# Kernel optimization log

Hardware: AMD Instinct MI355X
Metric: run time of the kernel (lower is better)

The kernel has to match this reference:

```python
import jax, jax.numpy as jnp
import numpy as np

D_MODEL = 1024
N_HEADS = 16  # long-term branch; short/medium use N_HEADS // 2


def _band_bias(seq_len, scale_factor):
    # Intended semantics of create_temporal_mask: position i may attend to
    # positions j >= i - scale_factor (recent past + all future); positions
    # further than scale_factor in the past are blocked.
    i = jnp.arange(seq_len)[:, None]
    j = jnp.arange(seq_len)[None, :]
    return jnp.where(j >= i - scale_factor, 0.0, -1e9).astype(jnp.float32)


def _mha(x, w_in, b_in, w_out, b_out, n_heads, bias):
    # Faithful nn.MultiheadAttention (batch_first, eval/no dropout).
    B, S, D = x.shape
    dk = D // n_heads
    qkv = x @ w_in.T + b_in                       # [B,S,3D]
    q, k, v = jnp.split(qkv, 3, axis=-1)
    def heads(t):
        return t.reshape(B, S, n_heads, dk).transpose(0, 2, 1, 3)  # [B,H,S,dk]
    q, k, v = heads(q), heads(k), heads(v)
    scores = jnp.einsum('bhid,bhjd->bhij', q, k) / np.sqrt(dk).astype(np.float32)
    if bias is not None:
        scores = scores + bias
    attn = jax.nn.softmax(scores, axis=-1)        # [B,H,S,S]
    out = jnp.einsum('bhij,bhjd->bhid', attn, v)  # [B,H,S,dk]
    out = out.transpose(0, 2, 1, 3).reshape(B, S, D)
    return out @ w_out.T + b_out, attn


def _layernorm(x, gamma, beta, eps=1e-5):
    mu = jnp.mean(x, axis=-1, keepdims=True)
    var = jnp.var(x, axis=-1, keepdims=True)
    return (x - mu) * jax.lax.rsqrt(var + eps) * gamma + beta


def setup_inputs() -> dict:
    key = jax.random.key(0)
    ks = jax.random.split(key, 12)
    D = D_MODEL
    s = 0.02
    inp = {
        'x': jax.random.normal(ks[0], (2, 2048, D), dtype=jnp.float32),
        'w_in_s': jax.random.normal(ks[1], (3 * D, D), dtype=jnp.float32) * s,
        'b_in_s': jnp.zeros((3 * D,), dtype=jnp.float32),
        'wo_s': jax.random.normal(ks[2], (D, D), dtype=jnp.float32) * s,
        'bo_s': jnp.zeros((D,), dtype=jnp.float32),
        'w_in_m': jax.random.normal(ks[3], (3 * D, D), dtype=jnp.float32) * s,
        'b_in_m': jnp.zeros((3 * D,), dtype=jnp.float32),
        'wo_m': jax.random.normal(ks[4], (D, D), dtype=jnp.float32) * s,
        'bo_m': jnp.zeros((D,), dtype=jnp.float32),
        'w_in_l': jax.random.normal(ks[5], (3 * D, D), dtype=jnp.float32) * s,
        'b_in_l': jnp.zeros((3 * D,), dtype=jnp.float32),
        'wo_l': jax.random.normal(ks[6], (D, D), dtype=jnp.float32) * s,
        'bo_l': jnp.zeros((D,), dtype=jnp.float32),
        'w_comb': jax.random.normal(ks[7], (D, 3 * D), dtype=jnp.float32) * s,
        'b_comb': jnp.zeros((D,), dtype=jnp.float32),
        'gamma': jnp.ones((D,), dtype=jnp.float32),
        'beta': jnp.zeros((D,), dtype=jnp.float32),
    }
    return inp


def reference(x, w_in_s, b_in_s, wo_s, bo_s,
              w_in_m, b_in_m, wo_m, bo_m,
              w_in_l, b_in_l, wo_l, bo_l,
              w_comb, b_comb, gamma, beta):
    B, S, D = x.shape
    short_bias = _band_bias(S, 10)
    medium_bias = _band_bias(S, 30)
    short_out, _ = _mha(x, w_in_s, b_in_s, wo_s, bo_s, N_HEADS // 2, short_bias)
    medium_out, _ = _mha(x, w_in_m, b_in_m, wo_m, bo_m, N_HEADS // 2, medium_bias)
    long_out, attn = _mha(x, w_in_l, b_in_l, wo_l, bo_l, N_HEADS, None)
    attn_weights = jnp.mean(attn, axis=1)  # torch default average_attn_weights=True -> [B,S,S]
    combined = jnp.concatenate([short_out, medium_out, long_out], axis=-1)
    output = combined @ w_comb.T + b_comb
    return _layernorm(output + x, gamma, beta), attn_weights
```

## Files before the change

kernel.cpp:

```cpp
#include <hip/hip_runtime.h>
#include <hip/hip_bf16.h>
#include <math.h>

#define B_ 2
#define S_ 2048
#define D_ 1024
#define M_ (B_*S_)
#define CTXLD 3072

typedef _Float16 half8_t __attribute__((ext_vector_type(8)));
typedef _Float16 half4_t __attribute__((ext_vector_type(4)));
typedef float    f32x4  __attribute__((ext_vector_type(4)));

#define GL2LDS(g, l) __builtin_amdgcn_global_load_lds( \
    (const __attribute__((address_space(1))) void*)(uintptr_t)(g), \
    (__attribute__((address_space(3))) void*)(l), 16, 0, 0)

#define QSC_L  0.18033688011112043f
#define QSC_SM 0.12751744653921766f

struct GemmBatch {
    const _Float16* A;
    const _Float16* W;
    const float*    bias;
    void*           C;
    void*           C2;
};

template<int MODE, int NB>
__device__ __forceinline__ void gemm_body(
    _Float16* As, _Float16* Bs, const GemmBatch& G,
    int lda, int ldw, int ldc, int K, int bx, int by, int bz)
{
    constexpr int NT = NB / 32;

    const int t = threadIdx.x, lane = t & 63, w = t >> 6;
    const int bm = bx * 128, bn = by * NB;
    const int wm = (w >> 1) * 64, wn = (w & 1) * (NB/2);
    const int fr = lane & 15, q8 = (lane >> 4) * 8;
    const int srow = lane >> 2, scol = (lane & 3) * 8;

    f32x4 acc[4][NT] = {};

    const _Float16* Ab = G.A + (size_t)(bm + w*32 + srow) * lda + scol;
    const _Float16* Wb = G.W + (size_t)(bn + w*(NB/4) + srow) * ldw + scol;

    for (int k0 = 0; k0 < K; k0 += 64) {
        __syncthreads();
        #pragma unroll
        for (int kc = 0; kc < 2; kc++) {
            #pragma unroll
            for (int ii = 0; ii < 2; ii++)
                GL2LDS(Ab + (size_t)(ii*16)*lda + k0 + kc*32,
                       As + kc*4096 + w*1024 + ii*512);
            #pragma unroll
            for (int ii = 0; ii < NB/64; ii++)
                GL2LDS(Wb + (size_t)(ii*16)*ldw + k0 + kc*32,
                       Bs + kc*NB*32 + w*(NB/4)*32 + ii*512);
        }
        __syncthreads();
        #pragma unroll
        for (int kc = 0; kc < 2; kc++) {
            half8_t af[4], bf[NT];
            #pragma unroll
            for (int mt = 0; mt < 4; mt++)
                af[mt] = *(const half8_t*)&As[kc*4096 + (wm + mt*16 + fr)*32 + q8];
            #pragma unroll
            for (int nt = 0; nt < NT; nt++)
                bf[nt] = *(const half8_t*)&Bs[kc*NB*32 + (wn + nt*16 + fr)*32 + q8];
            #pragma unroll
            for (int mt = 0; mt < 4; mt++)
                #pragma unroll
                for (int nt = 0; nt < NT; nt++)
                    acc[mt][nt] = __builtin_amdgcn_mfma_f32_16x16x32_f16(
                        af[mt], bf[nt], acc[mt][nt], 0, 0, 0);
        }
    }

    const int cl = lane & 15;
    const int rq = (lane >> 4) * 4;

    if (MODE == 2 && bn >= 2048) {
        #pragma unroll
        for (int mt = 0; mt < 4; mt++) {
            int row0 = bm + wm + mt*16 + rq;
            #pragma unroll
            for (int nt = 0; nt < NT; nt++) {
                int gcol = bn + wn + nt*16 + cl;
                float bv = G.bias[gcol];
                half4_t hv = {(_Float16)(acc[mt][nt][0] + bv),
                              (_Float16)(acc[mt][nt][1] + bv),
                              (_Float16)(acc[mt][nt][2] + bv),
                              (_Float16)(acc[mt][nt][3] + bv)};
                *(half4_t*)((_Float16*)G.C2 + (size_t)(gcol - 2048) * M_ + row0) = hv;
            }
        }
        return;
    }

    const float qsc = (MODE == 2 && bn < 1024)
                      ? ((bz == 2) ? QSC_L : QSC_SM) : 1.0f;

    #pragma unroll
    for (int mt = 0; mt < 4; mt++) {
        #pragma unroll
        for (int r = 0; r < 4; r++) {
            size_t grow = (size_t)(bm + wm + mt*16 + rq + r);
            #pragma unroll
            for (int nt = 0; nt < NT; nt++) {
                int gcol = bn + wn + nt*16 + cl;
                float v = acc[mt][nt][r] + ((MODE == 3) ? 0.f : G.bias[gcol]);
                if (MODE == 2) v *= qsc;
                if (MODE == 0)
                    ((float*)G.C)[grow * ldc + gcol] = v;
                else
                    ((_Float16*)G.C)[grow * ldc + gcol] = (_Float16)v;
            }
        }
    }
}

template<int MODE, int NB>
__global__ __launch_bounds__(256) void gemm_f16(
    GemmBatch b0, GemmBatch b1, GemmBatch b2, int lda, int ldw, int ldc, int K)
{
    __shared__ __align__(16) _Float16 As[2*128*32];
    __shared__ __align__(16) _Float16 Bs[2*NB*32];
    const GemmBatch G = (blockIdx.z == 0) ? b0 : ((blockIdx.z == 1) ? b1 : b2);
    gemm_body<MODE, NB>(As, Bs, G, lda, ldw, ldc, K,
                        blockIdx.x, blockIdx.y, blockIdx.z);
}

struct CastArgs {
    const float* s[5];
    _Float16*    d[5];
    int          nb[5];
};

__global__ __launch_bounds__(256) void prep_mega(
    CastArgs a,
    const float* wo_s, const float* wo_m, const float* wo_l,
    _Float16* woT_s, _Float16* woT_m, _Float16* woT_l,
    const float* __restrict__ w_comb, const float* __restrict__ b_comb,
    const float* __restrict__ bo_s, const float* __restrict__ bo_m,
    const float* __restrict__ bo_l, float* __restrict__ beff)
{
    __shared__ float T[64][68];
    __shared__ float red[4];
    const int bid = blockIdx.x;

    if (bid < 16384) {
        int off = bid;
        int seg = 0;
        while (seg < 4 && off >= a.nb[seg]) { off -= a.nb[seg]; seg++; }
        int i = off * 256 + threadIdx.x;
        float4 v = ((const float4*)a.s[seg])[i];
        half4_t h = {(_Float16)v.x, (_Float16)v.y, (_Float16)v.z, (_Float16)v.w};
        ((half4_t*)a.d[seg])[i] = h;
        return;
    }
    if (bid < 16384 + 768) {
        int rr0 = bid - 16384;
        int bz = rr0 >> 8, rem = rr0 & 255;
        int bx = rem & 15, by = rem >> 4;
        const float* src = bz == 0 ? wo_s : (bz == 1 ? wo_m : wo_l);
        _Float16*    dst = bz == 0 ? woT_s : (bz == 1 ? woT_m : woT_l);
        const int db = bx * 64;
        const int eb = by * 64;
        const int r = threadIdx.x >> 4;
        const int c = (threadIdx.x & 15) * 4;

        #pragma unroll
        for (int rr = 0; rr < 4; rr++) {
            float4 v = *(const float4*)&src[(size_t)(db + rr*16 + r)*1024 + eb + c];
            T[rr*16 + r][c+0] = v.x; T[rr*16 + r][c+1] = v.y;
            T[rr*16 + r][c+2] = v.z; T[rr*16 + r][c+3] = v.w;
        }
        __syncthreads();
        #pragma unroll
        for (int rr = 0; rr < 4; rr++) {
            int e = rr*16 + r;
            half4_t hv = {(_Float16)T[c+0][e], (_Float16)T[c+1][e],
                          (_Float16)T[c+2][e], (_Float16)T[c+3][e]};
            *(half4_t*)&dst[(size_t)(eb + e)*1024 + db + c] = hv;
        }
        return;
    }
    {
        const int n = bid - (16384 + 768), t = threadIdx.x;
        float s = 0.f;
        for (int d = t; d < 1024; d += 256)
            s += w_comb[(size_t)n*3072 + d]        * bo_s[d]
               + w_comb[(size_t)n*3072 + 1024 + d] * bo_m[d]
               + w_comb[(size_t)n*3072 + 2048 + d] * bo_l[d];
        #pragma unroll
        for (int m = 32; m >= 1; m >>= 1) s += __shfl_xor(s, m);
        if ((t & 63) == 0) red[t >> 6] = s;
        __syncthreads();
        if (t == 0) beff[n] = b_comb[n] + red[0] + red[1] + red[2] + red[3];
    }
}

template<int DK, int BJ, bool LOUT>
__device__ __forceinline__ void flash_body(
    _Float16* lds, float* Lw,
    const _Float16* __restrict__ qk, const _Float16* __restrict__ vT,
    _Float16* __restrict__ ctx, float* __restrict__ lout,
    int window, int b, int h, int qblk, int H)
{
    constexpr int KS  = DK / 32;
    constexpr int DT  = DK / 16;
    constexpr int JT  = BJ / 16;
    constexpr int JC  = BJ / 32;
    constexpr int LDP = 40;

    _Float16* Ks = lds;
    _Float16* Vs = lds + DK*BJ;
    _Float16* Ps = lds + 2*DK*BJ;

    const int t = threadIdx.x, lane = t & 63, w = t >> 6;
    const int fr = lane & 15, g = lane >> 4, k8 = g * 8;
    const int k8s = (g ^ ((fr >> 1) & 3)) * 8;
    const int blkQ = qblk * 64;
    const int qlo  = blkQ + w * 16;

    _Float16* PsW = Ps + w * 16 * LDP;
    const int srow = lane >> 2;
    const int ssw  = ((lane & 3) ^ ((srow >> 1) & 3)) * 8;

    half8_t qf[KS];
    #pragma unroll
    for (int kk = 0; kk < KS; kk++)
        qf[kk] = *(const half8_t*)&qk[(size_t)(b*S_ + qlo + fr)*2048 + h*DK + kk*32 + k8];

    f32x4 O[DT] = {};
    float lsum = 0.f;

    for (int j0 = 0; j0 < S_; j0 += BJ) {
        if (window >= 0 && j0 + BJ - 1 < blkQ - window) continue;
        __syncthreads();

        #pragma unroll
        for (int kk = 0; kk < KS; kk++)
            #pragma unroll
            for (int ii = 0; ii < BJ/64; ii++)
                GL2LDS(&qk[(size_t)(b*S_ + j0 + w*(BJ/4) + ii*16 + srow)*2048
                           + 1024 + h*DK + kk*32 + ssw],
                       &Ks[kk*BJ*32 + w*(BJ/4)*32 + ii*512]);
        #pragma unroll
        for (int jc = 0; jc < JC; jc++)
            #pragma unroll
            for (int ii = 0; ii < DK/64; ii++)
                GL2LDS(&vT[(size_t)(h*DK + w*(DK/4) + ii*16 + srow)*M_
                           + b*S_ + j0 + jc*32 + ssw],
                       &Vs[jc*DK*32 + w*(DK/4)*32 + ii*512]);
        __syncthreads();

        f32x4 st[JT];
        #pragma unroll
        for (int jt = 0; jt < JT; jt++) {
            f32x4 s = {};
            #pragma unroll
            for (int kk = 0; kk < KS; kk++) {
                half8_t kf = *(const half8_t*)&Ks[kk*BJ*32 + (jt*16 + fr)*32 + k8s];
                s = __builtin_amdgcn_mfma_f32_16x16x32_f16(kf, qf[kk], s, 0, 0, 0);
            }
            st[jt] = s;
        }

        const bool full = (window < 0) || (j0 >= qlo + 15 - window);
        #pragma unroll
        for (int kc = 0; kc < JC; kc++) {
            #pragma unroll
            for (int jh = 0; jh < 2; jh++) {
                int jt = kc*2 + jh;
                float p[4];
                #pragma unroll
                for (int r = 0; r < 4; r++) {
                    float pv = exp2f(st[jt][r]);
                    if (!full) {
                        int jg = j0 + jt*16 + g*4 + r;
                        if (jg < (qlo + fr) - window) pv = 0.f;
                    }
                    p[r] = pv;
                    lsum += pv;
                }
                half4_t ph = {(_Float16)p[0], (_Float16)p[1],
                              (_Float16)p[2], (_Float16)p[3]};
                *(half4_t*)&PsW[fr*LDP + jh*16 + g*4] = ph;
            }
            half8_t pf = *(const half8_t*)&PsW[fr*LDP + k8];
            #pragma unroll
            for (int dt = 0; dt < DT; dt++) {
                half8_t vf = *(const half8_t*)&Vs[kc*DK*32 + (dt*16 + fr)*32 + k8s];
                O[dt] = __builtin_amdgcn_mfma_f32_16x16x32_f16(pf, vf, O[dt], 0, 0, 0);
            }
        }
    }

    lsum += __shfl_xor(lsum, 16);
    lsum += __shfl_xor(lsum, 32);
    if (g == 0) Lw[w*16 + fr] = lsum;
    float linv[4];
    #pragma unroll
    for (int r = 0; r < 4; r++)
        linv[r] = 1.f / Lw[w*16 + g*4 + r];

    if (LOUT && g == 0)
        lout[(size_t)(b*H + h)*S_ + qlo + fr] = lsum;

    #pragma unroll
    for (int r = 0; r < 4; r++) {
        _Float16* cp = ctx + (size_t)(b*S_ + qlo + g*4 + r)*CTXLD + h*DK;
        #pragma unroll
        for (int dt = 0; dt < DT; dt++)
            cp[dt*16 + fr] = (_Float16)(O[dt][r] * linv[r]);
    }
}

__global__ __launch_bounds__(256, 4) void flash_mega(
    const _Float16* __restrict__ qk_s, const _Float16* __restrict__ qk_m,
    const _Float16* __restrict__ qk_l,
    const _Float16* __restrict__ vT_s, const _Float16* __restrict__ vT_m,
    const _Float16* __restrict__ vT_l,
    _Float16* __restrict__ ctxall, float* __restrict__ lbuf)
{
    __shared__ __align__(16) _Float16 lds[18944];
    __shared__ float Lw[64];

    const int hwb = blockIdx.x;
    const int bid = (hwb & 7) * 256 + (hwb >> 3);
    if (bid < 1024) {
        int qblk = bid & 31, h = (bid >> 5) & 15, b = bid >> 9;
        flash_body<64, 128, true>(lds, Lw, qk_l, vT_l, ctxall + 2048, lbuf,
                                  -1, b, h, qblk, 16);
    } else {
        int r = bid - 1024;
        int qblk = r & 31;
        int h = (r >> 5) & 7;
        int z = r >> 8;
        int br = z >> 1, b = z & 1;
        flash_body<128, 64, false>(lds, Lw, br ? qk_m : qk_s, br ? vT_m : vT_s,
                                   ctxall + (br ? 1024 : 0), nullptr,
                                   br ? 30 : 10, b, h, qblk, 8);
    }
}

__device__ __forceinline__ void attn_mean_body(
    _Float16* Ks,
    const _Float16* __restrict__ qk,
    const float* __restrict__ lbuf,
    float* __restrict__ attn, int bx, int by, int b)
{
    const int t = threadIdx.x, lane = t & 63, w = t >> 6;
    const int fr = lane & 15, g = lane >> 4, k8 = g * 8;
    const int k8s = (g ^ ((fr >> 1) & 3)) * 8;
    const int j0 = bx * 128;
    const int irow = by * 64 + w * 16;
    const int srow = lane >> 2;
    const int ssw  = ((lane & 3) ^ ((srow >> 1) & 3)) * 8;

    f32x4 acc[8] = {};

    for (int hp = 0; hp < 16; hp += 2) {
        __syncthreads();
        #pragma unroll
        for (int hh = 0; hh < 2; hh++)
            #pragma unroll
            for (int kk = 0; kk < 2; kk++)
                #pragma unroll
                for (int ii = 0; ii < 2; ii++)
                    GL2LDS(&qk[(size_t)(b*S_ + j0 + w*32 + ii*16 + srow)*2048
                               + 1024 + (hp+hh)*64 + kk*32 + ssw],
                           &Ks[hh*8192 + kk*4096 + w*1024 + ii*512]);
        __syncthreads();

        #pragma unroll
        for (int hh = 0; hh < 2; hh++) {
            const int h = hp + hh;
            half8_t af[2];
            #pragma unroll
            for (int kk = 0; kk < 2; kk++)
                af[kk] = *(const half8_t*)
                    &qk[(size_t)(b*S_ + irow + fr)*2048 + h*64 + kk*32 + k8];

            float lg[4];
            #pragma unroll
            for (int r = 0; r < 4; r++)
                lg[r] = __log2f(lbuf[(size_t)(b*16 + h)*S_ + irow + g*4 + r]) + 4.0f;

            #pragma unroll
            for (int nt = 0; nt < 8; nt++) {
                f32x4 s = {};
                #pragma unroll
                for (int kk = 0; kk < 2; kk++) {
                    half8_t bf = *(const half8_t*)
                        &Ks[hh*8192 + kk*4096 + (nt*16 + fr)*32 + k8s];
                    s = __builtin_amdgcn_mfma_f32_16x16x32_f16(af[kk], bf, s, 0, 0, 0);
                }
                #pragma unroll
                for (int r = 0; r < 4; r++)
                    acc[nt][r] += exp2f(s[r] - lg[r]);
            }
        }
    }

    #pragma unroll
    for (int r = 0; r < 4; r++) {
        float* p = attn + (size_t)(b*S_ + irow + g*4 + r)*S_ + j0;
        #pragma unroll
        for (int nt = 0; nt < 8; nt++)
            p[nt*16 + fr] = acc[nt][r];
    }
}

__global__ __launch_bounds__(256, 4) void tail_mega(
    GemmBatch fb, const _Float16* __restrict__ qk_l,
    const float* __restrict__ lbuf, float* __restrict__ attn_o)
{
    __shared__ __align__(16) _Float16 lds[16384];

    const int bid = blockIdx.x;
    if (bid < 512) {
        gemm_body<0, 64>(lds, lds + 8192, fb,
                         3072, 3072, D_, 3072, bid & 31, bid >> 5, 0);
    } else {
        int r = bid - 512;
        attn_mean_body(lds, qk_l, lbuf, attn_o,
                       r & 15, (r >> 4) & 31, r >> 9);
    }
}

__global__ __launch_bounds__(256) void ln_residual(
    const float* __restrict__ pre, const float* __restrict__ x,
    const float* __restrict__ gamma, const float* __restrict__ beta,
    float* __restrict__ out)
{
    __shared__ float redS[4], redQ[4];
    const int row = blockIdx.x;
    const int t = threadIdx.x;
    size_t base = (size_t)row * D_ + t * 4;

    float4 v  = *(const float4*)(pre + base);
    float4 xv = *(const float4*)(x + base);
    v.x += xv.x; v.y += xv.y; v.z += xv.z; v.w += xv.w;

    float s = v.x + v.y + v.z + v.w;
    float q = v.x*v.x + v.y*v.y + v.z*v.z + v.w*v.w;
    #pragma unroll
    for (int m = 32; m >= 1; m >>= 1) {
        s += __shfl_xor(s, m);
        q += __shfl_xor(q, m);
    }
    int wave = t >> 6;
    if ((t & 63) == 0) { redS[wave] = s; redQ[wave] = q; }
    __syncthreads();
    s = redS[0] + redS[1] + redS[2] + redS[3];
    q = redQ[0] + redQ[1] + redQ[2] + redQ[3];

    float mean = s * (1.f / D_);
    float var  = q * (1.f / D_) - mean * mean;
    float rstd = rsqrtf(var + 1e-5f);

    float4 g  = *(const float4*)(gamma + t * 4);
    float4 be = *(const float4*)(beta + t * 4);
    float4 o;
    o.x = (v.x - mean) * rstd * g.x + be.x;
    o.y = (v.y - mean) * rstd * g.y + be.y;
    o.z = (v.z - mean) * rstd * g.z + be.z;
    o.w = (v.w - mean) * rstd * g.w + be.w;
    *(float4*)(out + base) = o;
}

extern "C" void kernel_launch(void* const* d_in, const int* in_sizes, int n_in,
                              void* d_out, int out_size, void* d_ws, size_t ws_size,
                              hipStream_t stream)
{
    (void)in_sizes; (void)n_in; (void)out_size; (void)ws_size;
    const float* x      = (const float*)d_in[0];
    const float* w_in_s = (const float*)d_in[1];
    const float* b_in_s = (const float*)d_in[2];
    const float* wo_s   = (const float*)d_in[3];
    const float* bo_s   = (const float*)d_in[4];
    const float* w_in_m = (const float*)d_in[5];
    const float* b_in_m = (const float*)d_in[6];
    const float* wo_m   = (const float*)d_in[7];
    const float* bo_m   = (const float*)d_in[8];
    const float* w_in_l = (const float*)d_in[9];
    const float* b_in_l = (const float*)d_in[10];
    const float* wo_l   = (const float*)d_in[11];
    const float* bo_l   = (const float*)d_in[12];
    const float* w_comb = (const float*)d_in[13];
    const float* b_comb = (const float*)d_in[14];
    const float* gamma  = (const float*)d_in[15];
    const float* beta   = (const float*)d_in[16];

    float* out    = (float*)d_out;
    float* attn_o = out + (size_t)M_ * D_;

    char* W = (char*)d_ws;
    _Float16* w_in_s_h = (_Float16*)(W);
    _Float16* w_in_m_h = (_Float16*)(W + 6291456);
    _Float16* w_in_l_h = (_Float16*)(W + 12582912);
    _Float16* w_comb_h = (_Float16*)(W + 18874368);
    _Float16* woT_s    = (_Float16*)(W + 25165824);
    _Float16* woT_m    = (_Float16*)(W + 27262976);
    _Float16* woT_l    = (_Float16*)(W + 29360128);
    _Float16* weff     = (_Float16*)(W + 31457280);
    _Float16* qk_s     = (_Float16*)(W + 37748736);
    _Float16* qk_m     = (_Float16*)(W + 54525952);
    _Float16* qk_l     = (_Float16*)(W + 71303168);
    _Float16* vT_s     = (_Float16*)(W + 88080384);
    _Float16* vT_m     = (_Float16*)(W + 96468992);
    _Float16* ctxall   = (_Float16*)(W + 104857600);
    _Float16* x_h      = (_Float16*)(W + 130023424);
    float*    lbuf     = (float*)   (W + 138412032);
    float*    beff     = (float*)   (W + 138674432);
    _Float16* vT_l     = w_comb_h;
    float*    pre      = (float*)qk_m;

    dim3 blk(256);
    GemmBatch nil = { nullptr, nullptr, nullptr, nullptr, nullptr };

    CastArgs ca;
    ca.s[0]=x;      ca.d[0]=x_h;      ca.nb[0]=4096;
    ca.s[1]=w_in_s; ca.d[1]=w_in_s_h; ca.nb[1]=3072;
    ca.s[2]=w_in_m; ca.d[2]=w_in_m_h; ca.nb[2]=3072;
    ca.s[3]=w_in_l; ca.d[3]=w_in_l_h; ca.nb[3]=3072;
    ca.s[4]=w_comb; ca.d[4]=w_comb_h; ca.nb[4]=3072;
    prep_mega<<<dim3(16384 + 768 + 1024), blk, 0, stream>>>(
        ca, wo_s, wo_m, wo_l, woT_s, woT_m, woT_l,
        w_comb, b_comb, bo_s, bo_m, bo_l, beff);

    GemmBatch we0 = { w_comb_h + 0,    woT_s, nullptr, weff + 0,    nullptr };
    GemmBatch we1 = { w_comb_h + 1024, woT_m, nullptr, weff + 1024, nullptr };
    GemmBatch we2 = { w_comb_h + 2048, woT_l, nullptr, weff + 2048, nullptr };
    gemm_f16<3, 64><<<dim3(8, 16, 3), blk, 0, stream>>>(we0, we1, we2, 3072, 1024, 3072, 1024);

    GemmBatch qs = { x_h, w_in_s_h, b_in_s, qk_s, vT_s };
    GemmBatch qm = { x_h, w_in_m_h, b_in_m, qk_m, vT_m };
    GemmBatch ql = { x_h, w_in_l_h, b_in_l, qk_l, vT_l };
    gemm_f16<2, 128><<<dim3(M_/128, 3072/128, 3), blk, 0, stream>>>(qs, qm, ql, D_, D_, 2048, D_);

    flash_mega<<<dim3(2048), blk, 0, stream>>>(
        qk_s, qk_m, qk_l, vT_s, vT_m, vT_l, ctxall, lbuf);

    GemmBatch fb = { ctxall, weff, beff, pre, nullptr };
    tail_mega<<<dim3(512 + 1024), blk, 0, stream>>>(fb, qk_l, lbuf, attn_o);

    ln_residual<<<dim3(M_), blk, 0, stream>>>(pre, x, gamma, beta, out);
}
```

Measured before the change: 517.7 us.

## Double flash-attention query block to 128 rows with 512-thread blocks

```diff
diff --git a/kernel.cpp b/kernel.cpp
--- a/kernel.cpp
+++ b/kernel.cpp
@@ -213,6 +213,8 @@
     constexpr int JT  = BJ / 16;
     constexpr int JC  = BJ / 32;
     constexpr int LDP = 40;
+    constexpr int KRB = BJ / 16;
+    constexpr int VRB = DK / 16;
 
     _Float16* Ks = lds;
     _Float16* Vs = lds + DK*BJ;
@@ -221,7 +223,7 @@
     const int t = threadIdx.x, lane = t & 63, w = t >> 6;
     const int fr = lane & 15, g = lane >> 4, k8 = g * 8;
     const int k8s = (g ^ ((fr >> 1) & 3)) * 8;
-    const int blkQ = qblk * 64;
+    const int blkQ = qblk * 128;
     const int qlo  = blkQ + w * 16;
 
     _Float16* PsW = Ps + w * 16 * LDP;
@@ -241,19 +243,21 @@
         __syncthreads();
 
         #pragma unroll
-        for (int kk = 0; kk < KS; kk++)
-            #pragma unroll
-            for (int ii = 0; ii < BJ/64; ii++)
-                GL2LDS(&qk[(size_t)(b*S_ + j0 + w*(BJ/4) + ii*16 + srow)*2048
-                           + 1024 + h*DK + kk*32 + ssw],
-                       &Ks[kk*BJ*32 + w*(BJ/4)*32 + ii*512]);
-        #pragma unroll
-        for (int jc = 0; jc < JC; jc++)
-            #pragma unroll
-            for (int ii = 0; ii < DK/64; ii++)
-                GL2LDS(&vT[(size_t)(h*DK + w*(DK/4) + ii*16 + srow)*M_
-                           + b*S_ + j0 + jc*32 + ssw],
-                       &Vs[jc*DK*32 + w*(DK/4)*32 + ii*512]);
+        for (int i = 0; i < 2; i++) {
+            int u = w*2 + i;
+            int kk = u / KRB, rb = u % KRB;
+            GL2LDS(&qk[(size_t)(b*S_ + j0 + rb*16 + srow)*2048
+                       + 1024 + h*DK + kk*32 + ssw],
+                   &Ks[kk*BJ*32 + rb*512]);
+        }
+        #pragma unroll
+        for (int i = 0; i < 2; i++) {
+            int u = w*2 + i;
+            int jc = u / VRB, rb = u % VRB;
+            GL2LDS(&vT[(size_t)(h*DK + rb*16 + srow)*M_
+                       + b*S_ + j0 + jc*32 + ssw],
+                   &Vs[jc*DK*32 + rb*512]);
+        }
         __syncthreads();
 
         f32x4 st[JT];
@@ -318,31 +322,31 @@
     }
 }
 
-__global__ __launch_bounds__(256, 4) void flash_mega(
+__global__ __launch_bounds__(512, 4) void flash_mega(
     const _Float16* __restrict__ qk_s, const _Float16* __restrict__ qk_m,
     const _Float16* __restrict__ qk_l,
     const _Float16* __restrict__ vT_s, const _Float16* __restrict__ vT_m,
     const _Float16* __restrict__ vT_l,
     _Float16* __restrict__ ctxall, float* __restrict__ lbuf)
 {
-    __shared__ __align__(16) _Float16 lds[18944];
-    __shared__ float Lw[64];
+    __shared__ __align__(16) _Float16 lds[21504];
+    __shared__ float Lw[128];
 
     const int hwb = blockIdx.x;
-    const int bid = (hwb & 7) * 256 + (hwb >> 3);
-    if (bid < 1024) {
-        int qblk = bid & 31, h = (bid >> 5) & 15, b = bid >> 9;
+    const int bid = (hwb & 7) * 128 + (hwb >> 3);
+    const int grp = bid >> 4, q = bid & 15;
+    if (!(grp & 1)) {
+        int lg = grp >> 1;
+        int b = lg >> 4, h = lg & 15;
         flash_body<64, 128, true>(lds, Lw, qk_l, vT_l, ctxall + 2048, lbuf,
-                                  -1, b, h, qblk, 16);
+                                  -1, b, h, q, 16);
     } else {
-        int r = bid - 1024;
-        int qblk = r & 31;
-        int h = (r >> 5) & 7;
-        int z = r >> 8;
-        int br = z >> 1, b = z & 1;
+        int sg = grp >> 1;
+        int z = sg >> 3;
+        int br = z >> 1, b = z & 1, h = sg & 7;
         flash_body<128, 64, false>(lds, Lw, br ? qk_m : qk_s, br ? vT_m : vT_s,
                                    ctxall + (br ? 1024 : 0), nullptr,
-                                   br ? 30 : 10, b, h, qblk, 8);
+                                   br ? 30 : 10, b, h, q, 8);
     }
 }
 
@@ -542,7 +546,7 @@
     GemmBatch ql = { x_h, w_in_l_h, b_in_l, qk_l, vT_l };
     gemm_f16<2, 128><<<dim3(M_/128, 3072/128, 3), blk, 0, stream>>>(qs, qm, ql, D_, D_, 2048, D_);
 
-    flash_mega<<<dim3(2048), blk, 0, stream>>>(
+    flash_mega<<<dim3(1024), dim3(512), 0, stream>>>(
         qk_s, qk_m, qk_l, vT_s, vT_m, vT_l, ctxall, lbuf);
 
     GemmBatch fb = { ctxall, weff, beff, pre, nullptr };
```

Measured after the change: 519.5 us. About the same (+0.3%).
